# Kernel tuning notes

Hardware: AMD Instinct MI355X
Metric: run time of the kernel (lower is better)

The kernel has to match this reference:

```python
import jax, jax.numpy as jnp
import numpy as np

DIM = 1024
HIDDEN = 2816
NUM_EXPERTS = 8
TOP_K = 2
BATCH, SEQ = 4, 2048


def setup_inputs() -> dict:
    key = jax.random.key(0)
    ks = jax.random.split(key, 5)
    x = jax.random.normal(ks[0], (BATCH, SEQ, DIM), dtype=jnp.float32)
    gate_w = jax.random.normal(ks[1], (NUM_EXPERTS, DIM), dtype=jnp.float32) * 0.02
    w1 = jax.random.normal(ks[2], (NUM_EXPERTS, HIDDEN, DIM), dtype=jnp.float32) * 0.02
    w3 = jax.random.normal(ks[3], (NUM_EXPERTS, HIDDEN, DIM), dtype=jnp.float32) * 0.02
    w2 = jax.random.normal(ks[4], (NUM_EXPERTS, DIM, HIDDEN), dtype=jnp.float32) * 0.02
    return {"x": x, "gate_w": gate_w, "w1": w1, "w3": w3, "w2": w2}


def reference(x, gate_w, w1, w3, w2):
    orig_shape = x.shape
    xf = x.reshape(-1, x.shape[-1])                      # [T, D]
    T = xf.shape[0]
    E, K = gate_w.shape[0], TOP_K

    # gating: softmax over experts, then top-k (descending, matches torch.topk)
    scores = jax.nn.softmax(xf @ gate_w.T, axis=-1)      # [T, E]
    expert_weights, expert_indices = jax.lax.top_k(scores, K)  # [T, K]
    expert_weights = expert_weights / jnp.sum(expert_weights, axis=-1, keepdims=True)

    # dispatch: each token duplicated K times (torch repeat_interleave)
    x_rep = jnp.repeat(xf, K, axis=0)                    # [T*K, D]
    flat_idx = expert_indices.reshape(-1)                # [T*K]

    # per-expert masked SwiGLU FFN, combined into y (loop over small fixed E)
    y = jnp.zeros_like(x_rep)
    for e in range(E):
        m = (flat_idx == e)[:, None]
        xe = jnp.where(m, x_rep, 0.0)                    # zero non-routed tokens
        h = jax.nn.silu(xe @ w1[e].T) * (xe @ w3[e].T)   # [T*K, H]
        out = h @ w2[e].T                                # [T*K, D]
        y = y + jnp.where(m, out, 0.0)

    # weighted combine over the K slots
    y = jnp.sum(y.reshape(T, K, -1) * expert_weights[..., None], axis=1)
    return y.reshape(orig_shape)
```

## Files before the change

kernel.cpp:

```cpp
#include <hip/hip_runtime.h>
#include <hip/hip_bf16.h>

#define NTOK 8192
#define DIM 1024
#define HID 2816
#define NE 8
#define NSLOT (NTOK*2)
#define BM 128
#define BK 32
#define MAXMT (NSLOT/BM + NE)

typedef float f32x4 __attribute__((ext_vector_type(4)));
typedef __bf16 bf16x8 __attribute__((ext_vector_type(8)));
typedef __bf16 bf16x4 __attribute__((ext_vector_type(4)));

#define MFMA(a,b,c) __builtin_amdgcn_mfma_f32_16x16x32_bf16(a,b,c,0,0,0)
#define SWZ(r,g) (((r)<<5) + ((((g) ^ (((r)>>1)&3)))<<3))

__device__ __forceinline__ void cvt_st8(__bf16* d, f32x4 a, f32x4 b){
  bf16x8 v;
  v[0]=(__bf16)a.x; v[1]=(__bf16)a.y; v[2]=(__bf16)a.z; v[3]=(__bf16)a.w;
  v[4]=(__bf16)b.x; v[5]=(__bf16)b.y; v[6]=(__bf16)b.z; v[7]=(__bf16)b.w;
  *reinterpret_cast<bf16x8*>(d) = v;
}
__device__ __forceinline__ void gld_lds16(const void* g, void* l){
  __builtin_amdgcn_global_load_lds(
    (const __attribute__((address_space(1))) void*)g,
    (__attribute__((address_space(3))) void*)l, 16, 0, 0);
}
__device__ __forceinline__ int xcd_map(int orig, int nwg){
  int q = nwg>>3, rr = nwg&7, x = orig&7, o = orig>>3;
  return (x<rr ? x*(q+1) : rr*(q+1)+(x-rr)*q) + o;
}

__global__ __launch_bounds__(256) void k_cvt3(
    const float* __restrict__ s1, const float* __restrict__ s3,
    const float* __restrict__ s2, __bf16* __restrict__ d1,
    __bf16* __restrict__ d3, __bf16* __restrict__ d2, int* __restrict__ cnt)
{
  if(blockIdx.x==0 && threadIdx.x < NE) cnt[threadIdx.x] = 0;
  const int PB = (NE*HID*DIM/8)/256;
  int seg = blockIdx.x / PB;
  int i   = (blockIdx.x % PB)*256 + threadIdx.x;
  const float* src = (seg==0) ? s1 : (seg==1) ? s3 : s2;
  __bf16*      dst = (seg==0) ? d1 : (seg==1) ? d3 : d2;
  const f32x4* s = reinterpret_cast<const f32x4*>(src) + (size_t)i*2;
  f32x4 a = s[0], b = s[1];
  cvt_st8(dst + (size_t)i*8, a, b);
}

__global__ __launch_bounds__(256) void k_gate(const float* __restrict__ x,
    const float* __restrict__ gw, int* __restrict__ idxs,
    float* __restrict__ wt, int* __restrict__ cnt, __bf16* __restrict__ xb,
    float* __restrict__ y)
{
  __shared__ double part[8][8][4];
  __shared__ double lg[8][8];

  int tid = threadIdx.x;
  int tl = tid>>5, e = (tid>>2)&7, q = tid&3;
  int t  = blockIdx.x*8 + tl;

  const f32x4* x4 = reinterpret_cast<const f32x4*>(x)  + (size_t)t*256 + q*64;
  const f32x4* g4 = reinterpret_cast<const f32x4*>(gw) + e*256 + q*64;

  double s0 = 0.0, s1 = 0.0;
#pragma unroll 4
  for(int j=0;j<64;j+=2){
    f32x4 a0 = x4[j],   b0 = g4[j];
    f32x4 a1 = x4[j+1], b1 = g4[j+1];
    s0 += (double)a0.x*b0.x + (double)a0.y*b0.y
        + (double)a0.z*b0.z + (double)a0.w*b0.w;
    s1 += (double)a1.x*b1.x + (double)a1.y*b1.y
        + (double)a1.z*b1.z + (double)a1.w*b1.w;
  }
  part[tl][e][q] = s0 + s1;
  __syncthreads();
  if(q==0)
    lg[tl][e] = part[tl][e][0] + part[tl][e][1] + part[tl][e][2] + part[tl][e][3];
  __syncthreads();

  if(tid < 8){
    int tt = blockIdx.x*8 + tid;
    int i1=0; double m1=lg[tid][0];
#pragma unroll
    for(int k=1;k<NE;k++) if(lg[tid][k]>m1){ m1=lg[tid][k]; i1=k; }
    int i2=-1; double m2=-1e300;
#pragma unroll
    for(int k=0;k<NE;k++) if(k!=i1 && lg[tid][k]>m2){ m2=lg[tid][k]; i2=k; }
    float e2 = __expf((float)(m2-m1));
    float w0 = 1.f/(1.f+e2);
    idxs[2*tt]=i1; idxs[2*tt+1]=i2;
    wt[2*tt]=w0;   wt[2*tt+1]=e2*w0;
    atomicAdd(&cnt[i1],1); atomicAdd(&cnt[i2],1);
  }

  const f32x4* xs = reinterpret_cast<const f32x4*>(x) + (size_t)blockIdx.x*2048;
  __bf16* xo = xb + (size_t)blockIdx.x*8192;
#pragma unroll
  for(int k=0;k<4;k++){
    int c = k*256 + tid;
    cvt_st8(xo + (size_t)c*8, xs[2*c], xs[2*c+1]);
  }

  f32x4* yz = reinterpret_cast<f32x4*>(y) + (size_t)blockIdx.x*2048;
#pragma unroll
  for(int k=0;k<8;k++)
    yz[k*256 + tid] = f32x4{0.f,0.f,0.f,0.f};
}

__global__ void k_prep(const int* __restrict__ cnt, int* __restrict__ off,
                       int* __restrict__ mtp, int* __restrict__ cursor)
{
  if(threadIdx.x==0){
    int o=0, m=0; off[0]=0; mtp[0]=0;
    for(int e=0;e<NE;e++){
      cursor[e]=o; o += cnt[e]; off[e+1]=o;
      m += (cnt[e]+BM-1)/BM;  mtp[e+1]=m;
    }
  }
}

__global__ __launch_bounds__(256) void k_scatter(const int* __restrict__ idxs,
    int* __restrict__ cursor, int* __restrict__ order)
{
  int t = blockIdx.x*blockDim.x + threadIdx.x;
#pragma unroll
  for(int k=0;k<2;k++){
    int s = 2*t+k;
    int e = idxs[s];
    int p = atomicAdd(&cursor[e],1);
    order[p]=s;
  }
}

__global__ __launch_bounds__(512) void k_ffn1(
    const __bf16* __restrict__ xb, const __bf16* __restrict__ w1b,
    const __bf16* __restrict__ w3b, const int* __restrict__ off,
    const int* __restrict__ mtp, const int* __restrict__ order,
    __bf16* __restrict__ h)
{
  __shared__ __align__(16) __bf16 lA [2][BM*BK];
  __shared__ __align__(16) __bf16 lB1[2][BM*BK];
  __shared__ __align__(16) __bf16 lB3[2][BM*BK];

  const int NT = HID/128;
  int wg = xcd_map(blockIdx.x, MAXMT*NT);
  int mt = wg / NT, nt = wg % NT;
  if (mt >= mtp[NE]) return;
  int e = 0;
  while (mt >= mtp[e+1]) e++;
  int row0    = off[e] + (mt - mtp[e])*BM;
  int row_end = off[e+1];
  int n0      = nt*128;

  int tid = threadIdx.x, lane = tid&63;
  int srow = tid>>2;
  int scol = ((tid&3) ^ ((srow>>1)&3))<<3;
  int arow = min(row0 + srow, row_end-1);
  int tok  = order[arow] >> 1;
  const __bf16* gA  = xb  + (size_t)tok*DIM + scol;
  const __bf16* gB1 = w1b + (size_t)e*HID*DIM + (size_t)(n0+srow)*DIM + scol;
  const __bf16* gB3 = w3b + (size_t)e*HID*DIM + (size_t)(n0+srow)*DIM + scol;
  int ldso = (tid>>6)<<9;

  int wm = (tid>>6)>>2, wn = (tid>>6)&3;
  int fr = lane & 15, gq = lane>>4;

  f32x4 acc1[4][2], acc3[4][2];
#pragma unroll
  for(int m=0;m<4;m++)
#pragma unroll
    for(int n=0;n<2;n++){ acc1[m][n]=f32x4{0.f,0.f,0.f,0.f}; acc3[m][n]=f32x4{0.f,0.f,0.f,0.f}; }

  gld_lds16(gA,  &lA [0][ldso]);
  gld_lds16(gB1, &lB1[0][ldso]);
  gld_lds16(gB3, &lB3[0][ldso]);
  __syncthreads();

  const int NK = DIM/BK;
  int buf=0;
  for(int kt=0; kt<NK; kt++){
    if(kt+1<NK){
      gld_lds16(gA  + (kt+1)*BK, &lA [buf^1][ldso]);
      gld_lds16(gB1 + (kt+1)*BK, &lB1[buf^1][ldso]);
      gld_lds16(gB3 + (kt+1)*BK, &lB3[buf^1][ldso]);
    }
    bf16x8 av[4], bv[2], cv[2];
#pragma unroll
    for(int m=0;m<4;m++) av[m]=*reinterpret_cast<const bf16x8*>(&lA[buf][SWZ(wm*64+m*16+fr, gq)]);
#pragma unroll
    for(int n=0;n<2;n++){
      bv[n]=*reinterpret_cast<const bf16x8*>(&lB1[buf][SWZ(wn*32+n*16+fr, gq)]);
      cv[n]=*reinterpret_cast<const bf16x8*>(&lB3[buf][SWZ(wn*32+n*16+fr, gq)]);
    }
#pragma unroll
    for(int m=0;m<4;m++)
#pragma unroll
      for(int n=0;n<2;n++){
        acc1[m][n]=MFMA(av[m],bv[n],acc1[m][n]);
        acc3[m][n]=MFMA(av[m],cv[n],acc3[m][n]);
      }
    __syncthreads();
    buf^=1;
  }

#pragma unroll
  for(int m=0;m<4;m++){
    int rbase = row0 + wm*64 + m*16 + (gq<<2);
#pragma unroll
    for(int r=0;r<4;r++){
      if(rbase+r < row_end){
        __bf16* hp = h + (size_t)(rbase+r)*HID + n0 + wn*32 + fr;
#pragma unroll
        for(int n=0;n<2;n++){
          float u = acc1[m][n][r], v = acc3[m][n][r];
          hp[n*16] = (__bf16)( (u/(1.f+__expf(-u))) * v );
        }
      }
    }
  }
}

__global__ __launch_bounds__(256) void k_ffn2(
    const __bf16* __restrict__ h, const __bf16* __restrict__ w2b,
    const int* __restrict__ off, const int* __restrict__ mtp,
    const int* __restrict__ order, const float* __restrict__ wt,
    float* __restrict__ y)
{
  __shared__ __align__(16) __bf16 lA[2][128*BK];
  __shared__ __align__(16) __bf16 lB[2][128*BK];

  const int NT = DIM/128;
  int wg = xcd_map(blockIdx.x, MAXMT*NT);
  int mt = wg / NT, nt = wg % NT;
  if (mt >= mtp[NE]) return;
  int e = 0;
  while (mt >= mtp[e+1]) e++;
  int row0    = off[e] + (mt - mtp[e])*BM;
  int row_end = off[e+1];
  int n0      = nt*128;

  int tid = threadIdx.x, lane = tid&63, wave = tid>>6;
  int srow = tid>>2;
  int scol = ((tid&3) ^ ((srow>>1)&3))<<3;
  int hr0 = min(row0 + srow,      NSLOT-1);
  int hr1 = min(row0 + srow + 64, NSLOT-1);
  const __bf16* gA0 = h   + (size_t)hr0*HID + scol;
  const __bf16* gA1 = h   + (size_t)hr1*HID + scol;
  const __bf16* gB0 = w2b + (size_t)e*DIM*HID + (size_t)(n0+srow)*HID + scol;
  const __bf16* gB1 = w2b + (size_t)e*DIM*HID + (size_t)(n0+srow+64)*HID + scol;
  int ldso = wave<<9;

  int wm = wave>>1, wn = wave&1;
  int fr = lane&15, gq = lane>>4;

  f32x4 acc[4][4];
#pragma unroll
  for(int m=0;m<4;m++)
#pragma unroll
    for(int n=0;n<4;n++) acc[m][n]=f32x4{0.f,0.f,0.f,0.f};

  gld_lds16(gA0, &lA[0][ldso]);
  gld_lds16(gA1, &lA[0][2048+ldso]);
  gld_lds16(gB0, &lB[0][ldso]);
  gld_lds16(gB1, &lB[0][2048+ldso]);
  __syncthreads();

  const int NK = HID/BK;
  int buf=0;
  for(int kt=0; kt<NK; kt++){
    if(kt+1<NK){
      gld_lds16(gA0 + (kt+1)*BK, &lA[buf^1][ldso]);
      gld_lds16(gA1 + (kt+1)*BK, &lA[buf^1][2048+ldso]);
      gld_lds16(gB0 + (kt+1)*BK, &lB[buf^1][ldso]);
      gld_lds16(gB1 + (kt+1)*BK, &lB[buf^1][2048+ldso]);
    }
    bf16x8 av[4], bv[4];
#pragma unroll
    for(int m=0;m<4;m++) av[m]=*reinterpret_cast<const bf16x8*>(&lA[buf][SWZ(wm*64+m*16+fr, gq)]);
#pragma unroll
    for(int n=0;n<4;n++) bv[n]=*reinterpret_cast<const bf16x8*>(&lB[buf][SWZ(wn*64+n*16+fr, gq)]);
#pragma unroll
    for(int m=0;m<4;m++)
#pragma unroll
      for(int n=0;n<4;n++)
        acc[m][n]=MFMA(av[m],bv[n],acc[m][n]);
    __syncthreads();
    buf^=1;
  }

#pragma unroll
  for(int m=0;m<4;m++){
    int rbase = row0 + wm*64 + m*16 + (gq<<2);
#pragma unroll
    for(int r=0;r<4;r++){
      int p = rbase + r;
      if(p < row_end){
        int s = order[p];
        float wv = wt[s];
        float* yp = y + (size_t)(s>>1)*DIM + n0 + wn*64 + fr;
#pragma unroll
        for(int n=0;n<4;n++) atomicAdd(&yp[n*16], wv*acc[m][n][r]);
      }
    }
  }
}

extern "C" void kernel_launch(void* const* d_in, const int* in_sizes, int n_in,
                              void* d_out, int out_size, void* d_ws, size_t ws_size,
                              hipStream_t stream)
{
  const float* x  = (const float*)d_in[0];
  const float* gw = (const float*)d_in[1];
  const float* w1 = (const float*)d_in[2];
  const float* w3 = (const float*)d_in[3];
  const float* w2 = (const float*)d_in[4];
  float* y = (float*)d_out;
  char* ws = (char*)d_ws;

  int*   cnt    = (int*)(ws + 0);
  int*   off    = (int*)(ws + 64);
  int*   mtp    = (int*)(ws + 128);
  int*   cursor = (int*)(ws + 256);
  int*   idxs   = (int*)(ws + 320);
  float* wt     = (float*)(ws + 320 + 65536);
  int*   order  = (int*)(ws + 320 + 2*65536);
  __bf16* h     = (__bf16*)(ws + 262464);
  __bf16* xb    = (__bf16*)(ws + 262464 + 92274688ull);
  __bf16* w1b   = (__bf16*)(ws + 262464 + 92274688ull + 16777216ull);
  __bf16* w3b   = (__bf16*)(ws + 262464 + 92274688ull + 16777216ull + 46137344ull);
  __bf16* w2b   = (__bf16*)(ws + 262464 + 92274688ull + 16777216ull + 2*46137344ull);

  const int PB = (NE*HID*DIM/8)/256;

  k_cvt3   <<<3*PB, 256, 0, stream>>>(w1, w3, w2, w1b, w3b, w2b, cnt);
  k_gate   <<<NTOK/8, 256, 0, stream>>>(x, gw, idxs, wt, cnt, xb, y);
  k_prep   <<<1, 64, 0, stream>>>(cnt, off, mtp, cursor);
  k_scatter<<<NTOK/256, 256, 0, stream>>>(idxs, cursor, order);
  k_ffn1   <<<MAXMT*(HID/128), 512, 0, stream>>>(xb, w1b, w3b, off, mtp, order, h);
  k_ffn2   <<<MAXMT*(DIM/128), 256, 0, stream>>>(h, w2b, off, mtp, order, wt, y);
}
```

Measured before the change: 656.4 us.

## Double the M tile to 256 rows in both FFN GEMMs and split the ffn1 launch

Measured after the change: 807.1 us. 1.23x slower.

```diff
diff --git a/kernel.cpp b/kernel.cpp
--- a/kernel.cpp
+++ b/kernel.cpp
@@ -6,7 +6,7 @@
 #define HID 2816
 #define NE 8
 #define NSLOT (NTOK*2)
-#define BM 128
+#define BM 256
 #define BK 32
 #define MAXMT (NSLOT/BM + NE)
 
@@ -134,19 +134,19 @@
   }
 }
 
+#define NT_H 11
 __global__ __launch_bounds__(512) void k_ffn1(
     const __bf16* __restrict__ xb, const __bf16* __restrict__ w1b,
     const __bf16* __restrict__ w3b, const int* __restrict__ off,
     const int* __restrict__ mtp, const int* __restrict__ order,
-    __bf16* __restrict__ h)
+    __bf16* __restrict__ h, int nt_off)
 {
   __shared__ __align__(16) __bf16 lA [2][BM*BK];
-  __shared__ __align__(16) __bf16 lB1[2][BM*BK];
-  __shared__ __align__(16) __bf16 lB3[2][BM*BK];
-
-  const int NT = HID/128;
-  int wg = xcd_map(blockIdx.x, MAXMT*NT);
-  int mt = wg / NT, nt = wg % NT;
+  __shared__ __align__(16) __bf16 lB1[2][128*BK];
+  __shared__ __align__(16) __bf16 lB3[2][128*BK];
+
+  int wg = xcd_map(blockIdx.x, MAXMT*NT_H);
+  int mt = wg / NT_H, nt = nt_off + wg % NT_H;
   if (mt >= mtp[NE]) return;
   int e = 0;
   while (mt >= mtp[e+1]) e++;
@@ -154,48 +154,49 @@
   int row_end = off[e+1];
   int n0      = nt*128;
 
-  int tid = threadIdx.x, lane = tid&63;
-  int srow = tid>>2;
-  int scol = ((tid&3) ^ ((srow>>1)&3))<<3;
-  int arow = min(row0 + srow, row_end-1);
-  int tok  = order[arow] >> 1;
-  const __bf16* gA  = xb  + (size_t)tok*DIM + scol;
-  const __bf16* gB1 = w1b + (size_t)e*HID*DIM + (size_t)(n0+srow)*DIM + scol;
-  const __bf16* gB3 = w3b + (size_t)e*HID*DIM + (size_t)(n0+srow)*DIM + scol;
-  int ldso = (tid>>6)<<9;
-
-  int wm = (tid>>6)>>2, wn = (tid>>6)&3;
-  int fr = lane & 15, gq = lane>>4;
-
-  f32x4 acc1[4][2], acc3[4][2];
-#pragma unroll
-  for(int m=0;m<4;m++)
+  int tid = threadIdx.x, lane = tid&63, wave = tid>>6;
+  int sr = tid>>2;
+  int scol = ((tid&3) ^ ((sr>>1)&3))<<3;
+  int ar0 = min(row0 + sr,       row_end-1);
+  int ar1 = min(row0 + sr + 128, row_end-1);
+  const __bf16* a0  = xb  + (size_t)(order[ar0]>>1)*DIM + scol;
+  const __bf16* a1  = xb  + (size_t)(order[ar1]>>1)*DIM + scol;
+  const __bf16* gB1 = w1b + (size_t)e*HID*DIM + (size_t)(n0+sr)*DIM + scol;
+  const __bf16* gB3 = w3b + (size_t)e*HID*DIM + (size_t)(n0+sr)*DIM + scol;
+  int ldso = wave<<9;
+
+  int wm = wave>>2, wn = wave&3;
+  int fr = lane&15, gq = lane>>4;
+
+  f32x4 acc1[8][2], acc3[8][2];
+#pragma unroll
+  for(int m=0;m<8;m++)
 #pragma unroll
     for(int n=0;n<2;n++){ acc1[m][n]=f32x4{0.f,0.f,0.f,0.f}; acc3[m][n]=f32x4{0.f,0.f,0.f,0.f}; }
 
-  gld_lds16(gA,  &lA [0][ldso]);
-  gld_lds16(gB1, &lB1[0][ldso]);
-  gld_lds16(gB3, &lB3[0][ldso]);
+#define F1_STG(b, kt_) { \
+    gld_lds16(a0  + (kt_)*BK, &lA [b][ldso]); \
+    gld_lds16(a1  + (kt_)*BK, &lA [b][4096+ldso]); \
+    gld_lds16(gB1 + (kt_)*BK, &lB1[b][ldso]); \
+    gld_lds16(gB3 + (kt_)*BK, &lB3[b][ldso]); }
+
+  F1_STG(0, 0);
   __syncthreads();
 
   const int NK = DIM/BK;
   int buf=0;
   for(int kt=0; kt<NK; kt++){
-    if(kt+1<NK){
-      gld_lds16(gA  + (kt+1)*BK, &lA [buf^1][ldso]);
-      gld_lds16(gB1 + (kt+1)*BK, &lB1[buf^1][ldso]);
-      gld_lds16(gB3 + (kt+1)*BK, &lB3[buf^1][ldso]);
-    }
-    bf16x8 av[4], bv[2], cv[2];
-#pragma unroll
-    for(int m=0;m<4;m++) av[m]=*reinterpret_cast<const bf16x8*>(&lA[buf][SWZ(wm*64+m*16+fr, gq)]);
+    if(kt+1<NK) F1_STG(buf^1, kt+1);
+    bf16x8 av[8], bv[2], cv[2];
+#pragma unroll
+    for(int m=0;m<8;m++) av[m]=*reinterpret_cast<const bf16x8*>(&lA[buf][SWZ(wm*128+m*16+fr, gq)]);
 #pragma unroll
     for(int n=0;n<2;n++){
       bv[n]=*reinterpret_cast<const bf16x8*>(&lB1[buf][SWZ(wn*32+n*16+fr, gq)]);
       cv[n]=*reinterpret_cast<const bf16x8*>(&lB3[buf][SWZ(wn*32+n*16+fr, gq)]);
     }
 #pragma unroll
-    for(int m=0;m<4;m++)
+    for(int m=0;m<8;m++)
 #pragma unroll
       for(int n=0;n<2;n++){
         acc1[m][n]=MFMA(av[m],bv[n],acc1[m][n]);
@@ -204,10 +205,11 @@
     __syncthreads();
     buf^=1;
   }
-
-#pragma unroll
-  for(int m=0;m<4;m++){
-    int rbase = row0 + wm*64 + m*16 + (gq<<2);
+#undef F1_STG
+
+#pragma unroll
+  for(int m=0;m<8;m++){
+    int rbase = row0 + wm*128 + m*16 + (gq<<2);
 #pragma unroll
     for(int r=0;r<4;r++){
       if(rbase+r < row_end){
@@ -222,13 +224,13 @@
   }
 }
 
-__global__ __launch_bounds__(256) void k_ffn2(
+__global__ __launch_bounds__(512) void k_ffn2(
     const __bf16* __restrict__ h, const __bf16* __restrict__ w2b,
     const int* __restrict__ off, const int* __restrict__ mtp,
     const int* __restrict__ order, const float* __restrict__ wt,
     float* __restrict__ y)
 {
-  __shared__ __align__(16) __bf16 lA[2][128*BK];
+  __shared__ __align__(16) __bf16 lA[2][BM*BK];
   __shared__ __align__(16) __bf16 lB[2][128*BK];
 
   const int NT = DIM/128;
@@ -242,14 +244,13 @@
   int n0      = nt*128;
 
   int tid = threadIdx.x, lane = tid&63, wave = tid>>6;
-  int srow = tid>>2;
-  int scol = ((tid&3) ^ ((srow>>1)&3))<<3;
-  int hr0 = min(row0 + srow,      NSLOT-1);
-  int hr1 = min(row0 + srow + 64, NSLOT-1);
+  int sr = tid>>2;
+  int scol = ((tid&3) ^ ((sr>>1)&3))<<3;
+  int hr0 = min(row0 + sr,       NSLOT-1);
+  int hr1 = min(row0 + sr + 128, NSLOT-1);
   const __bf16* gA0 = h   + (size_t)hr0*HID + scol;
   const __bf16* gA1 = h   + (size_t)hr1*HID + scol;
-  const __bf16* gB0 = w2b + (size_t)e*DIM*HID + (size_t)(n0+srow)*HID + scol;
-  const __bf16* gB1 = w2b + (size_t)e*DIM*HID + (size_t)(n0+srow+64)*HID + scol;
+  const __bf16* gB  = w2b + (size_t)e*DIM*HID + (size_t)(n0+sr)*HID + scol;
   int ldso = wave<<9;
 
   int wm = wave>>1, wn = wave&1;
@@ -261,21 +262,18 @@
 #pragma unroll
     for(int n=0;n<4;n++) acc[m][n]=f32x4{0.f,0.f,0.f,0.f};
 
-  gld_lds16(gA0, &lA[0][ldso]);
-  gld_lds16(gA1, &lA[0][2048+ldso]);
-  gld_lds16(gB0, &lB[0][ldso]);
-  gld_lds16(gB1, &lB[0][2048+ldso]);
+#define F2_STG(b, kt_) { \
+    gld_lds16(gA0 + (kt_)*BK, &lA[b][ldso]); \
+    gld_lds16(gA1 + (kt_)*BK, &lA[b][4096+ldso]); \
+    gld_lds16(gB  + (kt_)*BK, &lB[b][ldso]); }
+
+  F2_STG(0, 0);
   __syncthreads();
 
   const int NK = HID/BK;
   int buf=0;
   for(int kt=0; kt<NK; kt++){
-    if(kt+1<NK){
-      gld_lds16(gA0 + (kt+1)*BK, &lA[buf^1][ldso]);
-      gld_lds16(gA1 + (kt+1)*BK, &lA[buf^1][2048+ldso]);
-      gld_lds16(gB0 + (kt+1)*BK, &lB[buf^1][ldso]);
-      gld_lds16(gB1 + (kt+1)*BK, &lB[buf^1][2048+ldso]);
-    }
+    if(kt+1<NK) F2_STG(buf^1, kt+1);
     bf16x8 av[4], bv[4];
 #pragma unroll
     for(int m=0;m<4;m++) av[m]=*reinterpret_cast<const bf16x8*>(&lA[buf][SWZ(wm*64+m*16+fr, gq)]);
@@ -289,6 +287,7 @@
     __syncthreads();
     buf^=1;
   }
+#undef F2_STG
 
 #pragma unroll
   for(int m=0;m<4;m++){
@@ -338,6 +337,7 @@
   k_gate   <<<NTOK/8, 256, 0, stream>>>(x, gw, idxs, wt, cnt, xb, y);
   k_prep   <<<1, 64, 0, stream>>>(cnt, off, mtp, cursor);
   k_scatter<<<NTOK/256, 256, 0, stream>>>(idxs, cursor, order);
-  k_ffn1   <<<MAXMT*(HID/128), 512, 0, stream>>>(xb, w1b, w3b, off, mtp, order, h);
-  k_ffn2   <<<MAXMT*(DIM/128), 256, 0, stream>>>(h, w2b, off, mtp, order, wt, y);
-}
+  k_ffn1   <<<MAXMT*NT_H, 512, 0, stream>>>(xb, w1b, w3b, off, mtp, order, h, 0);
+  k_ffn1   <<<MAXMT*NT_H, 512, 0, stream>>>(xb, w1b, w3b, off, mtp, order, h, NT_H);
+  k_ffn2   <<<MAXMT*(DIM/128), 512, 0, stream>>>(h, w2b, off, mtp, order, wt, y);
+}
```
